# Optimization experiments

Hardware: AMD Instinct MI355X
Metric: run time of the kernel (lower is better)

Reference implementation:

```python
import jax, jax.numpy as jnp
import numpy as np

NUM_EXPERTS = 8
IN_FEATURES = 1024
OUT_FEATURES = 1024
TOTAL_TOKENS = 8192


def setup_inputs() -> dict:
    key = jax.random.key(0)
    k_x, k_w, k_b = jax.random.split(key, 3)
    inputs = jax.random.normal(k_x, (TOTAL_TOKENS, IN_FEATURES), dtype=jnp.float32)
    # lecun_normal-style scale for the per-expert kernels
    kernel = jax.random.normal(k_w, (NUM_EXPERTS, IN_FEATURES, OUT_FEATURES), dtype=jnp.float32) / np.sqrt(IN_FEATURES)
    bias = jax.random.normal(k_b, (NUM_EXPERTS, OUT_FEATURES), dtype=jnp.float32) * 0.01
    # ragged group sizes that sum exactly to TOTAL_TOKENS (tokens pre-sorted by expert)
    rng = np.random.default_rng(0)
    gs = rng.multinomial(TOTAL_TOKENS, [1.0 / NUM_EXPERTS] * NUM_EXPERTS)
    group_sizes = jnp.asarray(gs, dtype=jnp.int32)
    return {"inputs": inputs, "group_sizes": group_sizes, "kernel": kernel, "bias": bias}


def reference(inputs, group_sizes, kernel, bias):
    # inputs: [T, in], kernel: [E, in, out], bias: [E, out], group_sizes: [E]
    E = kernel.shape[0]
    T = inputs.shape[0]
    # per-token expert id (tokens are sorted/grouped by expert)
    expert_ids = jnp.repeat(jnp.arange(E, dtype=jnp.int32), group_sizes, total_repeat_length=T)  # [T]
    onehot = jax.nn.one_hot(expert_ids, E, dtype=inputs.dtype)  # [T, E]
    # grouped ragged matmul: y[t] = x[t] @ W[expert_ids[t]]
    xe = jnp.einsum("te,ti->eti", onehot, inputs)  # [E, T, in], zero outside each expert's group
    y = jnp.einsum("eti,eio->to", xe, kernel)  # [T, out]
    # ragged bias expansion: bias of the owning expert per token
    y = y + jnp.take(bias, expert_ids, axis=0)
    return y
```

## Files before the change

### kernel.cpp

```cpp
#include <hip/hip_runtime.h>
#include <hip/hip_bf16.h>

#define T_TOK 8192
#define KDIM  1024
#define NDIM  1024
#define NEXP  8
#define LDA   40

typedef __bf16 bf16x8 __attribute__((ext_vector_type(8)));
typedef __bf16 bf16x4 __attribute__((ext_vector_type(4)));
typedef float  f32x4  __attribute__((ext_vector_type(4)));

__global__ __launch_bounds__(256) void moe_gemm_kernel(
    const float* __restrict__ x, const int* __restrict__ gs,
    const float* __restrict__ W, const float* __restrict__ bias,
    float* __restrict__ out)
{
  __shared__ __bf16 Al[128 * LDA];
  __shared__ __bf16 Bl[128 * LDA];

  const int e  = blockIdx.z;
  const int mt = blockIdx.y;
  const int nt = blockIdx.x;

  int off = 0;
#pragma unroll
  for (int i = 0; i < NEXP; ++i) { int g = gs[i]; if (i < e) off += g; }
  const int ge = gs[e];
  const int m0 = mt * 128;
  if (m0 >= ge) return;
  const int rows = min(128, ge - m0);
  const int row0 = off + m0;
  const int n0   = nt * 128;

  const int t    = threadIdx.x;
  const int lane = t & 63;
  const int wv   = t >> 6;
  const int wm   = wv & 1;
  const int wn   = wv >> 1;
  const int lm   = lane & 15;
  const int lg   = lane >> 4;

  const int am = t >> 3;
  const int kq = t & 7;
  const int nb = t & 127;
  const int kh = t >> 7;

  float4 aReg[4];
  float  bReg[16];

  const float* Wp = W + (size_t)e * KDIM * NDIM + n0 + nb;

  auto load_tile = [&](int kt) {
#pragma unroll
    for (int p = 0; p < 4; ++p) {
      int r = am + 32 * p;
      if (r < rows) {
        aReg[p] = *(const float4*)(x + (size_t)(row0 + r) * KDIM + kt * 32 + kq * 4);
      } else {
        aReg[p] = make_float4(0.f, 0.f, 0.f, 0.f);
      }
    }
    const float* wp = Wp + (size_t)(kt * 32 + kh * 16) * NDIM;
#pragma unroll
    for (int j = 0; j < 16; ++j) bReg[j] = wp[(size_t)j * NDIM];
  };

  auto store_tile = [&]() {
#pragma unroll
    for (int p = 0; p < 4; ++p) {
      bf16x4 v;
      v[0] = (__bf16)aReg[p].x; v[1] = (__bf16)aReg[p].y;
      v[2] = (__bf16)aReg[p].z; v[3] = (__bf16)aReg[p].w;
      *(bf16x4*)(Al + (am + 32 * p) * LDA + kq * 4) = v;
    }
    bf16x8 b0, b1;
#pragma unroll
    for (int j = 0; j < 8; ++j) { b0[j] = (__bf16)bReg[j]; b1[j] = (__bf16)bReg[8 + j]; }
    *(bf16x8*)(Bl + nb * LDA + kh * 16)     = b0;
    *(bf16x8*)(Bl + nb * LDA + kh * 16 + 8) = b1;
  };

  f32x4 acc[4][4] = {};

  load_tile(0);
#pragma unroll 1
  for (int kt = 0; kt < KDIM / 32; ++kt) {
    __syncthreads();
    store_tile();
    __syncthreads();
    if (kt + 1 < KDIM / 32) load_tile(kt + 1);

    bf16x8 af[4], bf[4];
#pragma unroll
    for (int i = 0; i < 4; ++i)
      af[i] = *(const bf16x8*)(Al + (wm * 64 + i * 16 + lm) * LDA + lg * 8);
#pragma unroll
    for (int j = 0; j < 4; ++j)
      bf[j] = *(const bf16x8*)(Bl + (wn * 64 + j * 16 + lm) * LDA + lg * 8);

#pragma unroll
    for (int i = 0; i < 4; ++i)
#pragma unroll
      for (int j = 0; j < 4; ++j)
        acc[i][j] = __builtin_amdgcn_mfma_f32_16x16x32_bf16(af[i], bf[j], acc[i][j], 0, 0, 0);
  }

  float bj[4];
#pragma unroll
  for (int j = 0; j < 4; ++j) bj[j] = bias[e * NDIM + n0 + wn * 64 + j * 16 + lm];

  float* op = out + (size_t)row0 * NDIM + n0;
#pragma unroll
  for (int i = 0; i < 4; ++i) {
#pragma unroll
    for (int r = 0; r < 4; ++r) {
      int rr = wm * 64 + i * 16 + lg * 4 + r;
      if (rr < rows) {
#pragma unroll
        for (int j = 0; j < 4; ++j)
          op[(size_t)rr * NDIM + wn * 64 + j * 16 + lm] = acc[i][j][r] + bj[j];
      }
    }
  }
}

extern "C" void kernel_launch(void* const* d_in, const int* in_sizes, int n_in,
                              void* d_out, int out_size, void* d_ws, size_t ws_size,
                              hipStream_t stream) {
  const float* x    = (const float*)d_in[0];
  const int*   gs   = (const int*)d_in[1];
  const float* W    = (const float*)d_in[2];
  const float* bias = (const float*)d_in[3];
  float*       out  = (float*)d_out;

  dim3 grid(NDIM / 128, T_TOK / 128, NEXP);
  moe_gemm_kernel<<<grid, 256, 0, stream>>>(x, gs, W, bias, out);
}
```

Before: 154.4 us.

## Add bf16 prepass with transposed weights and direct global-to-LDS loads

Adds a prepass kernel that converts the activations to bf16 and converts plus transposes the expert weights into a workspace laid out K-contiguous. The main GEMM then streams tiles with global_load_lds straight into shared memory, with no register staging or conversion, and uses a compacted grid that maps blocks only to valid expert row tiles. The goal is to cut strided fp32 weight loads and per-tile conversion work. In exchange it pays an extra pass over x and W, roughly 64MB of traffic, requires workspace, and drops the register prefetch overlap in the main loop.

Result: slower. 161.5 us (+4.6%).

```diff
diff --git a/kernel.cpp b/kernel.cpp
--- a/kernel.cpp
+++ b/kernel.cpp
@@ -1,15 +1,151 @@
 #include <hip/hip_runtime.h>
 #include <hip/hip_bf16.h>
 
-#define T_TOK 8192
-#define KDIM  1024
-#define NDIM  1024
-#define NEXP  8
-#define LDA   40
+#define KDIM 1024
+#define NDIM 1024
+#define NEXP 8
+#define TTOK 8192
+#define LDA  40
 
 typedef __bf16 bf16x8 __attribute__((ext_vector_type(8)));
 typedef __bf16 bf16x4 __attribute__((ext_vector_type(4)));
 typedef float  f32x4  __attribute__((ext_vector_type(4)));
+
+__device__ __forceinline__ void gl2lds16(const void* g, void* l) {
+  __builtin_amdgcn_global_load_lds(
+      (const __attribute__((address_space(1))) void*)g,
+      (__attribute__((address_space(3))) void*)l, 16, 0, 0);
+}
+
+__global__ __launch_bounds__(256) void prepass(
+    const float* __restrict__ x, const float* __restrict__ W,
+    __bf16* __restrict__ xb, __bf16* __restrict__ Wt)
+{
+  __shared__ __align__(16) __bf16 Lt[64 * 72];
+  const int t = threadIdx.x;
+  if (blockIdx.x < 1024) {
+    int gid = blockIdx.x * 256 + t;
+#pragma unroll
+    for (int p = 0; p < 4; ++p) {
+      size_t i8 = (size_t)(gid + p * 262144) * 8;
+      float4 a = *(const float4*)(x + i8);
+      float4 b = *(const float4*)(x + i8 + 4);
+      bf16x8 v;
+      v[0] = (__bf16)a.x; v[1] = (__bf16)a.y; v[2] = (__bf16)a.z; v[3] = (__bf16)a.w;
+      v[4] = (__bf16)b.x; v[5] = (__bf16)b.y; v[6] = (__bf16)b.z; v[7] = (__bf16)b.w;
+      *(bf16x8*)(xb + i8) = v;
+    }
+  } else {
+    int bid = blockIdx.x - 1024;
+    int e = bid >> 8, r = bid & 255;
+    int k0 = (r >> 4) * 64, n0 = (r & 15) * 64;
+    const float* Wp = W + (size_t)e * KDIM * NDIM;
+    int rr0 = t >> 4, c4 = t & 15;
+#pragma unroll
+    for (int p = 0; p < 4; ++p) {
+      int kk = rr0 + p * 16;
+      float4 v = *(const float4*)(Wp + (size_t)(k0 + kk) * NDIM + n0 + c4 * 4);
+      Lt[(c4 * 4 + 0) * 72 + kk] = (__bf16)v.x;
+      Lt[(c4 * 4 + 1) * 72 + kk] = (__bf16)v.y;
+      Lt[(c4 * 4 + 2) * 72 + kk] = (__bf16)v.z;
+      Lt[(c4 * 4 + 3) * 72 + kk] = (__bf16)v.w;
+    }
+    __syncthreads();
+    __bf16* Wte = Wt + (size_t)e * NDIM * KDIM;
+    int n = t >> 2, kq = t & 3;
+#pragma unroll
+    for (int q = 0; q < 2; ++q) {
+      int kqq = kq + q * 4;
+      bf16x8 v = *(const bf16x8*)(Lt + n * 72 + kqq * 8);
+      *(bf16x8*)(Wte + (size_t)(n0 + n) * KDIM + k0 + kqq * 8) = v;
+    }
+  }
+}
+
+__global__ __launch_bounds__(256) void moe_gemm_bf16(
+    const __bf16* __restrict__ xb, const __bf16* __restrict__ Wt,
+    const int* __restrict__ gs, const float* __restrict__ bias,
+    float* __restrict__ out)
+{
+  __shared__ __align__(16) __bf16 Al[4096];
+  __shared__ __align__(16) __bf16 Bl[4096];
+
+  int y = blockIdx.y;
+  int e = 0, row0 = 0, rows = 0, found = 0, off = 0;
+#pragma unroll
+  for (int i = 0; i < NEXP; ++i) {
+    int g = gs[i];
+    int tc = (g + 127) >> 7;
+    if (!found) {
+      if (y < tc) { found = 1; e = i; row0 = off + y * 128; rows = min(128, g - y * 128); }
+      else y -= tc;
+    }
+    off += g;
+  }
+  if (!found) return;
+  const int n0 = blockIdx.x * 128;
+
+  const int t = threadIdx.x, lane = t & 63, wv = t >> 6;
+  const int wm = wv & 1, wn = wv >> 1, lm = lane & 15, lg = lane >> 4;
+
+  const int c0 = wv * 2, c1 = wv * 2 + 1;
+  const int s0 = c0 * 64 + lane, s1 = c1 * 64 + lane;
+  const int r0 = s0 & 127, k0h = s0 >> 7;
+  const int r1 = s1 & 127, k1h = s1 >> 7;
+
+  const __bf16* gA0 = xb + (size_t)(row0 + r0) * KDIM + k0h * 8;
+  const __bf16* gA1 = xb + (size_t)(row0 + r1) * KDIM + k1h * 8;
+  const __bf16* Wte = Wt + (size_t)e * NDIM * KDIM;
+  const __bf16* gB0 = Wte + (size_t)(n0 + r0) * KDIM + k0h * 8;
+  const __bf16* gB1 = Wte + (size_t)(n0 + r1) * KDIM + k1h * 8;
+  __bf16* lA0 = Al + c0 * 512;
+  __bf16* lA1 = Al + c1 * 512;
+  __bf16* lB0 = Bl + c0 * 512;
+  __bf16* lB1 = Bl + c1 * 512;
+
+  f32x4 acc[4][4] = {};
+
+#pragma unroll 1
+  for (int kt = 0; kt < KDIM / 32; ++kt) {
+    const int ko = kt * 32;
+    gl2lds16(gA0 + ko, lA0);
+    gl2lds16(gA1 + ko, lA1);
+    gl2lds16(gB0 + ko, lB0);
+    gl2lds16(gB1 + ko, lB1);
+    __syncthreads();
+
+    bf16x8 af[4], bfr[4];
+#pragma unroll
+    for (int i = 0; i < 4; ++i)
+      af[i] = *(const bf16x8*)(Al + lg * 1024 + (wm * 64 + i * 16 + lm) * 8);
+#pragma unroll
+    for (int j = 0; j < 4; ++j)
+      bfr[j] = *(const bf16x8*)(Bl + lg * 1024 + (wn * 64 + j * 16 + lm) * 8);
+
+#pragma unroll
+    for (int i = 0; i < 4; ++i)
+#pragma unroll
+      for (int j = 0; j < 4; ++j)
+        acc[i][j] = __builtin_amdgcn_mfma_f32_16x16x32_bf16(af[i], bfr[j], acc[i][j], 0, 0, 0);
+    __syncthreads();
+  }
+
+  float bj[4];
+#pragma unroll
+  for (int j = 0; j < 4; ++j) bj[j] = bias[e * NDIM + n0 + wn * 64 + j * 16 + lm];
+  float* op = out + (size_t)row0 * NDIM + n0;
+#pragma unroll
+  for (int i = 0; i < 4; ++i)
+#pragma unroll
+    for (int r = 0; r < 4; ++r) {
+      int rr = wm * 64 + i * 16 + lg * 4 + r;
+      if (rr < rows) {
+#pragma unroll
+        for (int j = 0; j < 4; ++j)
+          op[(size_t)rr * NDIM + wn * 64 + j * 16 + lm] = acc[i][j][r] + bj[j];
+      }
+    }
+}
 
 __global__ __launch_bounds__(256) void moe_gemm_kernel(
     const float* __restrict__ x, const int* __restrict__ gs,
@@ -18,11 +154,7 @@
 {
   __shared__ __bf16 Al[128 * LDA];
   __shared__ __bf16 Bl[128 * LDA];
-
-  const int e  = blockIdx.z;
-  const int mt = blockIdx.y;
-  const int nt = blockIdx.x;
-
+  const int e = blockIdx.z, mt = blockIdx.y, nt = blockIdx.x;
   int off = 0;
 #pragma unroll
   for (int i = 0; i < NEXP; ++i) { int g = gs[i]; if (i < e) off += g; }
@@ -31,41 +163,23 @@
   if (m0 >= ge) return;
   const int rows = min(128, ge - m0);
   const int row0 = off + m0;
-  const int n0   = nt * 128;
-
-  const int t    = threadIdx.x;
-  const int lane = t & 63;
-  const int wv   = t >> 6;
-  const int wm   = wv & 1;
-  const int wn   = wv >> 1;
-  const int lm   = lane & 15;
-  const int lg   = lane >> 4;
-
-  const int am = t >> 3;
-  const int kq = t & 7;
-  const int nb = t & 127;
-  const int kh = t >> 7;
-
-  float4 aReg[4];
-  float  bReg[16];
-
+  const int n0 = nt * 128;
+  const int t = threadIdx.x, lane = t & 63, wv = t >> 6;
+  const int wm = wv & 1, wn = wv >> 1, lm = lane & 15, lg = lane >> 4;
+  const int am = t >> 3, kq = t & 7, nb = t & 127, kh = t >> 7;
+  float4 aReg[4]; float bReg[16];
   const float* Wp = W + (size_t)e * KDIM * NDIM + n0 + nb;
-
   auto load_tile = [&](int kt) {
 #pragma unroll
     for (int p = 0; p < 4; ++p) {
       int r = am + 32 * p;
-      if (r < rows) {
-        aReg[p] = *(const float4*)(x + (size_t)(row0 + r) * KDIM + kt * 32 + kq * 4);
-      } else {
-        aReg[p] = make_float4(0.f, 0.f, 0.f, 0.f);
-      }
+      if (r < rows) aReg[p] = *(const float4*)(x + (size_t)(row0 + r) * KDIM + kt * 32 + kq * 4);
+      else aReg[p] = make_float4(0.f, 0.f, 0.f, 0.f);
     }
     const float* wp = Wp + (size_t)(kt * 32 + kh * 16) * NDIM;
 #pragma unroll
     for (int j = 0; j < 16; ++j) bReg[j] = wp[(size_t)j * NDIM];
   };
-
   auto store_tile = [&]() {
 #pragma unroll
     for (int p = 0; p < 4; ++p) {
@@ -77,12 +191,10 @@
     bf16x8 b0, b1;
 #pragma unroll
     for (int j = 0; j < 8; ++j) { b0[j] = (__bf16)bReg[j]; b1[j] = (__bf16)bReg[8 + j]; }
-    *(bf16x8*)(Bl + nb * LDA + kh * 16)     = b0;
+    *(bf16x8*)(Bl + nb * LDA + kh * 16) = b0;
     *(bf16x8*)(Bl + nb * LDA + kh * 16 + 8) = b1;
   };
-
   f32x4 acc[4][4] = {};
-
   load_tile(0);
 #pragma unroll 1
   for (int kt = 0; kt < KDIM / 32; ++kt) {
@@ -90,29 +202,25 @@
     store_tile();
     __syncthreads();
     if (kt + 1 < KDIM / 32) load_tile(kt + 1);
-
-    bf16x8 af[4], bf[4];
+    bf16x8 af[4], bfr[4];
 #pragma unroll
     for (int i = 0; i < 4; ++i)
       af[i] = *(const bf16x8*)(Al + (wm * 64 + i * 16 + lm) * LDA + lg * 8);
 #pragma unroll
     for (int j = 0; j < 4; ++j)
-      bf[j] = *(const bf16x8*)(Bl + (wn * 64 + j * 16 + lm) * LDA + lg * 8);
-
+      bfr[j] = *(const bf16x8*)(Bl + (wn * 64 + j * 16 + lm) * LDA + lg * 8);
 #pragma unroll
     for (int i = 0; i < 4; ++i)
 #pragma unroll
       for (int j = 0; j < 4; ++j)
-        acc[i][j] = __builtin_amdgcn_mfma_f32_16x16x32_bf16(af[i], bf[j], acc[i][j], 0, 0, 0);
-  }
-
+        acc[i][j] = __builtin_amdgcn_mfma_f32_16x16x32_bf16(af[i], bfr[j], acc[i][j], 0, 0, 0);
+  }
   float bj[4];
 #pragma unroll
   for (int j = 0; j < 4; ++j) bj[j] = bias[e * NDIM + n0 + wn * 64 + j * 16 + lm];
-
   float* op = out + (size_t)row0 * NDIM + n0;
 #pragma unroll
-  for (int i = 0; i < 4; ++i) {
+  for (int i = 0; i < 4; ++i)
 #pragma unroll
     for (int r = 0; r < 4; ++r) {
       int rr = wm * 64 + i * 16 + lg * 4 + r;
@@ -122,7 +230,6 @@
           op[(size_t)rr * NDIM + wn * 64 + j * 16 + lm] = acc[i][j][r] + bj[j];
       }
     }
-  }
 }
 
 extern "C" void kernel_launch(void* const* d_in, const int* in_sizes, int n_in,
@@ -134,6 +241,14 @@
   const float* bias = (const float*)d_in[3];
   float*       out  = (float*)d_out;
 
-  dim3 grid(NDIM / 128, T_TOK / 128, NEXP);
-  moe_gemm_kernel<<<grid, 256, 0, stream>>>(x, gs, W, bias, out);
-}
+  const size_t xb_bytes = (size_t)TTOK * KDIM * 2;
+  const size_t wt_bytes = (size_t)NEXP * KDIM * NDIM * 2;
+  if (ws_size >= xb_bytes + wt_bytes) {
+    __bf16* xb = (__bf16*)d_ws;
+    __bf16* Wt = (__bf16*)((char*)d_ws + xb_bytes);
+    prepass<<<dim3(1024 + 2048), 256, 0, stream>>>(x, W, xb, Wt);
+    moe_gemm_bf16<<<dim3(NDIM / 128, 72), 256, 0, stream>>>(xb, Wt, gs, bias, out);
+  } else {
+    moe_gemm_kernel<<<dim3(NDIM / 128, TTOK / 128, NEXP), 256, 0, stream>>>(x, gs, W, bias, out);
+  }
+}
```
